# Performance work log

Measured on AMD Instinct MI355X. Metric: run time of the kernel, lower is better.

Reference implementation:

```python
import jax, jax.numpy as jnp
import numpy as np

K = 4  # spline order (degree K-1)


def bspline_basis(x, t, k):
    """Evaluate the k nonzero B-spline basis functions of order k at x.

    x: [B, I] floats; t: [G+2k-1] clamped knot vector.
    Returns (idx [B,I,k] int32 basis indices, basis [B,I,k] values),
    using the de Boor / NURBS-book triangular recursion (vectorized over B,I;
    Python loops only over the small fixed order k).
    """
    m = t.shape[0]
    # interval index: t[i] <= x < t[i+1], clamped to valid span [k-1, m-k-1]
    i = jnp.clip(jnp.searchsorted(t, x, side='right') - 1, k - 1, m - k - 1)
    p = k - 1
    N = [jnp.ones_like(x)]
    left, right = [], []
    for j in range(1, p + 1):
        left.append(x - t[i + 1 - j])
        right.append(t[i + j] - x)
        saved = jnp.zeros_like(x)
        Nn = []
        for r in range(j):
            temp = N[r] / (right[r] + left[j - 1 - r])
            Nn.append(saved + right[r] * temp)
            saved = left[j - 1 - r] * temp
        Nn.append(saved)
        N = Nn
    idx = jnp.stack([i - p + j for j in range(k)], axis=-1)   # [B,I,k]
    basis = jnp.stack(N, axis=-1)                             # [B,I,k]
    return idx, basis


def setup_inputs() -> dict:
    key = jax.random.key(0)
    k1, k2 = jax.random.split(key)
    B, I, O, G, k = 2048, 128, 128, 64, K
    t0, t1 = -1.0, 1.0
    x = jax.random.uniform(k1, (B, I), jnp.float32, minval=t0, maxval=t1)
    # xavier_normal_ for fan_in=in_dim, fan_out=out_dim (per-slice heuristic)
    std = (2.0 / (I + O)) ** 0.5
    w = jax.random.normal(k2, (G + k, I, O), jnp.float32) * std
    t = jnp.concatenate([
        jnp.full((k - 1,), t0, jnp.float32),
        jnp.linspace(t0, t1, G + 1, dtype=jnp.float32),
        jnp.full((k - 1,), t1, jnp.float32),
    ])
    return {"x": x, "w": w, "t": t}


def reference(x, w, t):
    k = K
    B, I = x.shape
    O = w.shape[2]
    idx, basis = bspline_basis(x, t, k)                       # [B,I,k]
    # activation slot uses the last row of w (torch index -1)
    act_idx = jnp.full((B, I, 1), w.shape[0] - 1, idx.dtype)
    idx_full = jnp.concatenate([idx, act_idx], axis=-1)       # [B,I,k+1]
    y = jnp.concatenate([basis, jax.nn.silu(x)[..., None]], axis=-1)  # [B,I,k+1]
    wt = jnp.transpose(w, (1, 0, 2))                          # [I, G+k, O]
    w2 = wt[jnp.arange(I)[None, :, None], idx_full]           # [B,I,k+1,O] gather
    return jnp.einsum('bij,bijo->bo', y, w2)                  # [B,O]
```

## Files before the change

kernel.cpp:

```cpp
#include <hip/hip_runtime.h>
#include <math.h>

#define B_TOTAL 2048
#define I_DIM   128
#define O_DIM   128
#define GK      68
#define NKNOT   71
#define BT      64
#define RI      8
#define NR      (I_DIM / RI)
#define THREADS 512
#define SLICE_FLOATS (GK * O_DIM)
#define CHUNKS  (SLICE_FLOATS / 256)
#define WS_NEED ((size_t)NR * B_TOTAL * O_DIM * 4)

__device__ __forceinline__ float rdlanef(float v, int l) {
    return __int_as_float(__builtin_amdgcn_readlane(__float_as_int(v), l));
}

template<bool USE_WS>
__global__ __launch_bounds__(THREADS, 4)
void flashkan_main(const float* __restrict__ x,
                   const float* __restrict__ w,
                   const float* __restrict__ t,
                   float* __restrict__ dst) {
    __shared__ float wbuf[2][SLICE_FLOATS];
    __shared__ float t_sh[NKNOT];

    const int tid  = threadIdx.x;
    const int bid  = blockIdx.x;
    const int bt   = bid >> 4;
    const int r    = bid & 15;
    const int b0   = bt * BT;
    const int i0   = r * RI;
    const int wave = tid >> 6;
    const int lane = tid & 63;

    if (tid < NKNOT) t_sh[tid] = t[tid];
    __syncthreads();

    float cf0, cf1, cf2, cf3, cf4;
    int   cg;
    {
        const int bl = lane >> 3;
        const int ii = lane & 7;
        const float xv = x[(size_t)(b0 + wave * 8 + bl) * I_DIM + (i0 + ii)];

        int ik = 3 + (int)floorf((xv + 1.0f) * 32.0f);
        ik = min(max(ik, 3), 66);
        while (ik < 66 && xv >= t_sh[ik + 1]) ++ik;
        while (ik > 3 && xv < t_sh[ik]) --ik;

        float l0, l1, l2, r0, r1, r2;
        float N0 = 1.0f, N1, N2, N3;
        l0 = xv - t_sh[ik];
        r0 = t_sh[ik + 1] - xv;
        {
            float temp = N0 / (r0 + l0);
            N0 = r0 * temp;
            N1 = l0 * temp;
        }
        l1 = xv - t_sh[ik - 1];
        r1 = t_sh[ik + 2] - xv;
        {
            float saved = 0.0f, temp;
            temp = N0 / (r0 + l1);
            N0 = saved + r0 * temp;
            saved = l1 * temp;
            temp = N1 / (r1 + l0);
            N1 = saved + r1 * temp;
            N2 = l0 * temp;
        }
        l2 = xv - t_sh[ik - 2];
        r2 = t_sh[ik + 3] - xv;
        {
            float saved = 0.0f, temp;
            temp = N0 / (r0 + l2);
            N0 = saved + r0 * temp;
            saved = l2 * temp;
            temp = N1 / (r1 + l1);
            N1 = saved + r1 * temp;
            saved = l1 * temp;
            temp = N2 / (r2 + l0);
            N2 = saved + r2 * temp;
            N3 = l0 * temp;
        }
        cf0 = N0; cf1 = N1; cf2 = N2; cf3 = N3;
        cf4 = xv / (1.0f + expf(-xv));
        cg  = ik - 3;
    }

    auto stage = [&](int sel, int i_abs) {
        for (int c = wave; c < CHUNKS; c += 8) {
            const int f = c * 256 + lane * 4;
            const int g = f >> 7;
            const int o = f & (O_DIM - 1);
            const float* src = w + ((size_t)g * I_DIM + i_abs) * O_DIM + o;
            void* dstp = (void*)&wbuf[sel][c * 256];
            __builtin_amdgcn_global_load_lds(
                (const __attribute__((address_space(1))) void*)src,
                (__attribute__((address_space(3))) void*)dstp,
                16, 0, 0);
        }
    };

    float2 acc[8];
    #pragma unroll
    for (int bl = 0; bl < 8; ++bl) acc[bl] = make_float2(0.0f, 0.0f);

    auto compute = [&](int ii, const float* buf) {
        const float2 v4 = ((const float2*)(buf + 67 * O_DIM))[lane];
        #pragma unroll
        for (int bl = 0; bl < 8; ++bl) {
            const int src = (bl << 3) | ii;
            const float c0 = rdlanef(cf0, src);
            const float c1 = rdlanef(cf1, src);
            const float c2 = rdlanef(cf2, src);
            const float c3 = rdlanef(cf3, src);
            const float c4 = rdlanef(cf4, src);
            const int   g0 = __builtin_amdgcn_readlane(cg, src);

            const float2* rp = (const float2*)(buf + (size_t)g0 * O_DIM) + lane;
            const float2 v0 = rp[0];
            const float2 v1 = rp[64];
            const float2 v2 = rp[128];
            const float2 v3 = rp[192];

            acc[bl].x += c0 * v0.x + c1 * v1.x + c2 * v2.x + c3 * v3.x + c4 * v4.x;
            acc[bl].y += c0 * v0.y + c1 * v1.y + c2 * v2.y + c3 * v3.y + c4 * v4.y;
        }
    };

    stage(0, i0);
    __syncthreads();

    for (int iib = 0; iib < RI; iib += 2) {
        stage(1, i0 + iib + 1);
        compute(iib, wbuf[0]);
        __syncthreads();
        if (iib + 2 < RI) stage(0, i0 + iib + 2);
        compute(iib + 1, wbuf[1]);
        __syncthreads();
    }

    #pragma unroll
    for (int bl = 0; bl < 8; ++bl) {
        const int b = b0 + wave * 8 + bl;
        if (USE_WS) {
            float2* dp = (float2*)(dst + ((size_t)r * B_TOTAL + b) * O_DIM) + lane;
            *dp = acc[bl];
        } else {
            atomicAdd(&dst[(size_t)b * O_DIM + 2 * lane],     acc[bl].x);
            atomicAdd(&dst[(size_t)b * O_DIM + 2 * lane + 1], acc[bl].y);
        }
    }
}

__global__ __launch_bounds__(256)
void flashkan_reduce(const float* __restrict__ ws, float* __restrict__ out) {
    const int f = blockIdx.x * 256 + threadIdx.x;
    const float4* base = (const float4*)ws + f;
    float4 s = make_float4(0.0f, 0.0f, 0.0f, 0.0f);
    #pragma unroll
    for (int r2 = 0; r2 < NR; ++r2) {
        const float4 v = base[(size_t)r2 * (B_TOTAL * O_DIM / 4)];
        s.x += v.x; s.y += v.y; s.z += v.z; s.w += v.w;
    }
    ((float4*)out)[f] = s;
}

extern "C" void kernel_launch(void* const* d_in, const int* in_sizes, int n_in,
                              void* d_out, int out_size, void* d_ws, size_t ws_size,
                              hipStream_t stream) {
    const float* x = (const float*)d_in[0];
    const float* w = (const float*)d_in[1];
    const float* t = (const float*)d_in[2];
    float* out = (float*)d_out;

    dim3 grid(32 * NR);
    dim3 block(THREADS);

    if (ws_size >= WS_NEED) {
        float* ws = (float*)d_ws;
        flashkan_main<true><<<grid, block, 0, stream>>>(x, w, t, ws);
        flashkan_reduce<<<B_TOTAL * O_DIM / 4 / 256, 256, 0, stream>>>(ws, out);
    } else {
        hipMemsetAsync(out, 0, (size_t)out_size * sizeof(float), stream);
        flashkan_main<false><<<grid, block, 0, stream>>>(x, w, t, out);
    }
}
```

Baseline: 31.95 us.

## Convert weights to bf16 and split basis terms across half-waves

A conversion kernel now runs first and writes the fp32 weights to bf16 in workspace. The main kernel stages the bf16 slices into LDS, which halves the LDS footprint and the staging traffic. Each half-wave takes two of the four basis rows over 4 output columns, and the halves are combined with a shuffle before the store. The cost is an extra launch plus a full pass over w on every call, and a loss of weight precision to bf16. The fallback path assumes the workspace can hold the bf16 copy but never checks its size.

Measured after the change: 42.21 us. 32.1% more time.

```diff
diff --git a/kernel.cpp b/kernel.cpp
--- a/kernel.cpp
+++ b/kernel.cpp
@@ -7,24 +7,42 @@
 #define GK      68
 #define NKNOT   71
 #define BT      64
+#define BTILES  (B_TOTAL / BT)
 #define RI      8
 #define NR      (I_DIM / RI)
 #define THREADS 512
-#define SLICE_FLOATS (GK * O_DIM)
-#define CHUNKS  (SLICE_FLOATS / 256)
-#define WS_NEED ((size_t)NR * B_TOTAL * O_DIM * 4)
+#define SLICE_ELEMS (GK * O_DIM)
+#define SLICE_BYTES (SLICE_ELEMS * 2)
+#define CHUNKS  (SLICE_BYTES / 1024)
+#define W_ELEMS ((size_t)GK * I_DIM * O_DIM)
+#define PART_FLOATS ((size_t)NR * B_TOTAL * O_DIM)
+#define WS_FULL (PART_FLOATS * 4 + W_ELEMS * 2)
+#define WS_MIN  (W_ELEMS * 2)
 
 __device__ __forceinline__ float rdlanef(float v, int l) {
     return __int_as_float(__builtin_amdgcn_readlane(__float_as_int(v), l));
+}
+__device__ __forceinline__ unsigned short f2bf(float f) {
+    unsigned u = __float_as_uint(f);
+    return (unsigned short)((u + 0x7fffu + ((u >> 16) & 1u)) >> 16);
+}
+
+__global__ __launch_bounds__(256)
+void wcvt(const float* __restrict__ w, unsigned short* __restrict__ wbf) {
+    const int e4 = blockIdx.x * 256 + threadIdx.x;
+    const float4 v = ((const float4*)w)[e4];
+    ushort4 o;
+    o.x = f2bf(v.x); o.y = f2bf(v.y); o.z = f2bf(v.z); o.w = f2bf(v.w);
+    ((ushort4*)wbf)[e4] = o;
 }
 
 template<bool USE_WS>
 __global__ __launch_bounds__(THREADS, 4)
 void flashkan_main(const float* __restrict__ x,
-                   const float* __restrict__ w,
+                   const unsigned short* __restrict__ wbf,
                    const float* __restrict__ t,
                    float* __restrict__ dst) {
-    __shared__ float wbuf[2][SLICE_FLOATS];
+    __shared__ unsigned short wbuf[2][SLICE_ELEMS];
     __shared__ float t_sh[NKNOT];
 
     const int tid  = threadIdx.x;
@@ -35,6 +53,8 @@
     const int i0   = r * RI;
     const int wave = tid >> 6;
     const int lane = tid & 63;
+    const int h    = lane >> 5;
+    const int loff = (lane & 31) << 3;
 
     if (tid < NKNOT) t_sh[tid] = t[tid];
     __syncthreads();
@@ -92,11 +112,11 @@
 
     auto stage = [&](int sel, int i_abs) {
         for (int c = wave; c < CHUNKS; c += 8) {
-            const int f = c * 256 + lane * 4;
-            const int g = f >> 7;
-            const int o = f & (O_DIM - 1);
-            const float* src = w + ((size_t)g * I_DIM + i_abs) * O_DIM + o;
-            void* dstp = (void*)&wbuf[sel][c * 256];
+            const int e = c * 512 + lane * 8;
+            const int g = e >> 7;
+            const int o = e & (O_DIM - 1);
+            const unsigned short* src = wbf + ((size_t)g * I_DIM + i_abs) * O_DIM + o;
+            void* dstp = (void*)((char*)&wbuf[sel][0] + c * 1024);
             __builtin_amdgcn_global_load_lds(
                 (const __attribute__((address_space(1))) void*)src,
                 (__attribute__((address_space(3))) void*)dstp,
@@ -104,30 +124,44 @@
         }
     };
 
-    float2 acc[8];
+    float4 acc[8];
     #pragma unroll
-    for (int bl = 0; bl < 8; ++bl) acc[bl] = make_float2(0.0f, 0.0f);
-
-    auto compute = [&](int ii, const float* buf) {
-        const float2 v4 = ((const float2*)(buf + 67 * O_DIM))[lane];
+    for (int bl = 0; bl < 8; ++bl) acc[bl] = make_float4(0.f, 0.f, 0.f, 0.f);
+
+    auto compute = [&](int ii, const unsigned short* buf) {
+        const char* bufc = (const char*)buf;
+        const uint2 u4 = *(const uint2*)(bufc + 67 * 256 + loff);
+        const float s0 = __uint_as_float(u4.x << 16);
+        const float s1 = __uint_as_float(u4.x & 0xffff0000u);
+        const float s2 = __uint_as_float(u4.y << 16);
+        const float s3 = __uint_as_float(u4.y & 0xffff0000u);
         #pragma unroll
         for (int bl = 0; bl < 8; ++bl) {
-            const int src = (bl << 3) | ii;
-            const float c0 = rdlanef(cf0, src);
-            const float c1 = rdlanef(cf1, src);
-            const float c2 = rdlanef(cf2, src);
-            const float c3 = rdlanef(cf3, src);
-            const float c4 = rdlanef(cf4, src);
-            const int   g0 = __builtin_amdgcn_readlane(cg, src);
-
-            const float2* rp = (const float2*)(buf + (size_t)g0 * O_DIM) + lane;
-            const float2 v0 = rp[0];
-            const float2 v1 = rp[64];
-            const float2 v2 = rp[128];
-            const float2 v3 = rp[192];
-
-            acc[bl].x += c0 * v0.x + c1 * v1.x + c2 * v2.x + c3 * v3.x + c4 * v4.x;
-            acc[bl].y += c0 * v0.y + c1 * v1.y + c2 * v2.y + c3 * v3.y + c4 * v4.y;
+            const int srcl = (bl << 3) | ii;
+            const float c0 = rdlanef(cf0, srcl);
+            const float c1 = rdlanef(cf1, srcl);
+            const float c2 = rdlanef(cf2, srcl);
+            const float c3 = rdlanef(cf3, srcl);
+            const float c4 = rdlanef(cf4, srcl);
+            const int   g0 = __builtin_amdgcn_readlane(cg, srcl);
+
+            const char* rp = bufc + ((g0 + h) << 8) + loff;
+            const uint2 uA = *(const uint2*)rp;
+            const uint2 uB = *(const uint2*)(rp + 512);
+
+            const float cA  = h ? c1 : c0;
+            const float cB  = h ? c3 : c2;
+            const float c4h = h ? 0.0f : c4;
+
+            float4& a = acc[bl];
+            a.x += cA * __uint_as_float(uA.x << 16)
+                 + cB * __uint_as_float(uB.x << 16)         + c4h * s0;
+            a.y += cA * __uint_as_float(uA.x & 0xffff0000u)
+                 + cB * __uint_as_float(uB.x & 0xffff0000u) + c4h * s1;
+            a.z += cA * __uint_as_float(uA.y << 16)
+                 + cB * __uint_as_float(uB.y << 16)         + c4h * s2;
+            a.w += cA * __uint_as_float(uA.y & 0xffff0000u)
+                 + cB * __uint_as_float(uB.y & 0xffff0000u) + c4h * s3;
         }
     };
 
@@ -145,13 +179,23 @@
 
     #pragma unroll
     for (int bl = 0; bl < 8; ++bl) {
+        float4 a = acc[bl];
+        a.x += __shfl(a.x, lane ^ 32);
+        a.y += __shfl(a.y, lane ^ 32);
+        a.z += __shfl(a.z, lane ^ 32);
+        a.w += __shfl(a.w, lane ^ 32);
         const int b = b0 + wave * 8 + bl;
-        if (USE_WS) {
-            float2* dp = (float2*)(dst + ((size_t)r * B_TOTAL + b) * O_DIM) + lane;
-            *dp = acc[bl];
-        } else {
-            atomicAdd(&dst[(size_t)b * O_DIM + 2 * lane],     acc[bl].x);
-            atomicAdd(&dst[(size_t)b * O_DIM + 2 * lane + 1], acc[bl].y);
+        if (lane < 32) {
+            if (USE_WS) {
+                float4* dp = (float4*)(dst + ((size_t)r * B_TOTAL + b) * O_DIM) + lane;
+                *dp = a;
+            } else {
+                float* dp = dst + (size_t)b * O_DIM + lane * 4;
+                atomicAdd(dp,     a.x);
+                atomicAdd(dp + 1, a.y);
+                atomicAdd(dp + 2, a.z);
+                atomicAdd(dp + 3, a.w);
+            }
         }
     }
 }
@@ -177,15 +221,19 @@
     const float* t = (const float*)d_in[2];
     float* out = (float*)d_out;
 
-    dim3 grid(32 * NR);
+    dim3 grid(BTILES * NR);
     dim3 block(THREADS);
 
-    if (ws_size >= WS_NEED) {
-        float* ws = (float*)d_ws;
-        flashkan_main<true><<<grid, block, 0, stream>>>(x, w, t, ws);
-        flashkan_reduce<<<B_TOTAL * O_DIM / 4 / 256, 256, 0, stream>>>(ws, out);
+    if (ws_size >= WS_FULL) {
+        float* part = (float*)d_ws;
+        unsigned short* wbf = (unsigned short*)((char*)d_ws + PART_FLOATS * 4);
+        wcvt<<<(int)(W_ELEMS / 4 / 256), 256, 0, stream>>>(w, wbf);
+        flashkan_main<true><<<grid, block, 0, stream>>>(x, wbf, t, part);
+        flashkan_reduce<<<B_TOTAL * O_DIM / 4 / 256, 256, 0, stream>>>(part, out);
     } else {
+        unsigned short* wbf = (unsigned short*)d_ws;
         hipMemsetAsync(out, 0, (size_t)out_size * sizeof(float), stream);
-        flashkan_main<false><<<grid, block, 0, stream>>>(x, w, t, out);
-    }
-}
+        wcvt<<<(int)(W_ELEMS / 4 / 256), 256, 0, stream>>>(w, wbf);
+        flashkan_main<false><<<grid, block, 0, stream>>>(x, wbf, t, out);
+    }
+}
```
